# Optimization experiments

Measured on AMD Instinct MI355X. Metric: run time of the kernel, lower is better.

The kernel has to match this reference:

```python
import jax, jax.numpy as jnp
import numpy as np

B, S, H, A = 32, 2048, 1024, 256
NEG = jnp.float32(-1e20)


def setup_inputs() -> dict:
    key = jax.random.key(0)
    k = jax.random.split(key, 6)
    h_i = jax.random.normal(k[0], (B, S, H), jnp.float32)
    h_t = jax.random.normal(k[1], (B, H), jnp.float32)
    mask = jax.random.randint(k[2], (B, S), 0, 2).astype(bool)
    W = jax.random.normal(k[3], (A, 2 * H), jnp.float32) * 0.02
    b = jax.random.normal(k[4], (A,), jnp.float32) * 0.02
    u = jax.random.normal(k[5], (A, 1), jnp.float32)
    return {"h_i": h_i, "h_t": h_t, "mask": mask, "W": W, "b": b, "u": u}


def reference(h_i, h_t, mask, W, b, u):
    Bn, Sn, Hn = h_i.shape
    # h_t expanded along seq and concatenated: [B,S,2H]
    h_t_e = jnp.broadcast_to(h_t[:, None, :], (Bn, Sn, Hn))
    comb = jnp.concatenate([h_i, h_t_e], axis=-1)
    m = jnp.tanh(jnp.einsum('bsk,ak->bsa', comb, W) + b)  # [B,S,A]
    y = jnp.einsum('bsa,a->bs', m, u[:, 0])                # raw scores [B,S]
    # Faithful replication of torch masked_scatter per time step over the batch
    # dim: at step s, the masked batch positions receive SUCCESSIVE elements of
    # the score column y[:, s] (not necessarily the positionally aligned ones).
    pos = jnp.clip(jnp.cumsum(mask.astype(jnp.int32), axis=0) - 1, 0)  # [B,S]
    y_scattered = jnp.take_along_axis(y, pos, axis=0)
    beta = jnp.where(mask, y_scattered, NEG)
    alpha = jax.nn.softmax(beta, axis=1)                   # softmax over seq
    s = jnp.einsum('bs,bsh->bh', alpha, h_i)               # weighted sum [B,H]
    return s
```

## Files before the change

kernel.cpp:

```cpp
#include <hip/hip_runtime.h>
#include <math.h>

#define BB 32
#define SS 2048
#define HH 1024
#define AA 256
#define NEGV (-1e20f)
#define BK 32
#define NT (HH / BK)
#define NG 16

typedef _Float16 half8 __attribute__((ext_vector_type(8)));
typedef float f32x4 __attribute__((ext_vector_type(4)));

__device__ inline void async_lds16(const void* g, void* l) {
    __builtin_amdgcn_global_load_lds(
        (const __attribute__((address_space(1))) unsigned int*)g,
        (__attribute__((address_space(3))) unsigned int*)l, 16, 0, 0);
}

__device__ inline f32x4 gload4(const float* p) {
    f32x4 r;
    asm volatile("global_load_dwordx4 %0, %1, off"
                 : "=&v"(r) : "v"(p) : "memory");
    return r;
}

__device__ inline half8 cvt8(f32x4 a, f32x4 b) {
    half8 h;
    h[0] = (_Float16)a[0]; h[1] = (_Float16)a[1];
    h[2] = (_Float16)a[2]; h[3] = (_Float16)a[3];
    h[4] = (_Float16)b[0]; h[5] = (_Float16)b[1];
    h[6] = (_Float16)b[2]; h[7] = (_Float16)b[3];
    return h;
}
__device__ inline half8 cvt8f(float4 a, float4 b) {
    half8 h;
    h[0] = (_Float16)a.x; h[1] = (_Float16)a.y;
    h[2] = (_Float16)a.z; h[3] = (_Float16)a.w;
    h[4] = (_Float16)b.x; h[5] = (_Float16)b.y;
    h[6] = (_Float16)b.z; h[7] = (_Float16)b.w;
    return h;
}

__global__ __launch_bounds__(256) void k_prep(const float* __restrict__ W,
                                              const float* __restrict__ h_t,
                                              const float* __restrict__ bias,
                                              const int* __restrict__ mask,
                                              _Float16* __restrict__ W16t,
                                              float* __restrict__ c,
                                              int* __restrict__ sList,
                                              int* __restrict__ cntb,
                                              int* __restrict__ pcnt) {
    const int blk = blockIdx.x;
    const int tid = threadIdx.x;
    __shared__ int lcnt;

    if (blk < 128) {
        int idx = blk * 256 + tid;
        int kt = idx >> 10;
        int u  = idx & 1023;
        int col = u >> 2, ks = u & 3;
        const float* src = W + (size_t)col * 2 * HH + kt * BK + ks * 8;
        float4 a0 = *(const float4*)src;
        float4 a1 = *(const float4*)(src + 4);
        *reinterpret_cast<half8*>(W16t + (size_t)idx * 8) = cvt8f(a0, a1);
        return;
    }
    if (blk < 2176) {
        int wave = tid >> 6;
        int lane = tid & 63;
        int pair = (blk - 128) * 4 + wave;
        int b = pair >> 8;
        int a = pair & (AA - 1);
        const float* ht = h_t + (size_t)b * HH;
        const float* w2 = W + (size_t)a * 2 * HH + HH;
        float acc = 0.f;
        for (int k = lane; k < HH; k += 64)
            acc += ht[k] * w2[k];
        for (int off = 32; off; off >>= 1)
            acc += __shfl_down(acc, off, 64);
        if (lane == 0) c[pair] = acc + bias[a];
        return;
    }
    const int b = blk - 2176;
    const int lane = tid & 63;
    if (tid == 0) lcnt = 0;
    __syncthreads();
    int* lst = sList + b * SS;
#pragma unroll
    for (int i = 0; i < 8; ++i) {
        int s = tid + i * 256;
        int pref = 0, tot = 0;
#pragma unroll
        for (int bb = 0; bb < BB; ++bb) {
            int mv = (mask[bb * SS + s] != 0);
            tot += mv;
            if (bb <= b) pref += mv;
        }
        pcnt[b * SS + s] = pref;
        bool need = (tot > b);
        unsigned long long mk = __ballot(need);
        int wbase = 0;
        if (lane == 0) wbase = atomicAdd(&lcnt, __popcll(mk));
        wbase = __shfl(wbase, 0, 64);
        if (need) lst[wbase + __popcll(mk & ((1ull << lane) - 1))] = s;
    }
    __syncthreads();
    const int m = lcnt;
    if (tid == 0) cntb[b] = m;
    if (m > 0) {
        int padded = (m + 63) & ~63;
        int first = lst[0];
        for (int j = m + tid; j < padded; j += 256) lst[j] = first;
    }
}

__global__ __launch_bounds__(256, 3) void k2_mfma(const float* __restrict__ h_i,
                                                  const _Float16* __restrict__ W16t,
                                                  const float* __restrict__ c,
                                                  const float* __restrict__ u,
                                                  const int* __restrict__ sList,
                                                  const int* __restrict__ cntb,
                                                  float* __restrict__ y) {
    __shared__ _Float16 Alds[3][4][64][8];
    __shared__ _Float16 Blds[2][1024][8];
    __shared__ float c_s[AA], u_s[AA];
    __shared__ float red[2][64];
    __shared__ int s_idx[64];

    const int t = blockIdx.x;
    int b = -1, ti = 0, base = 0;
    for (int bb = 0; bb < BB; ++bb) {
        int nt = (cntb[bb] + 63) >> 6;
        if (b < 0 && t < base + nt) { b = bb; ti = t - base; }
        base += nt;
    }
    if (b < 0) return;

    const int tid = threadIdx.x;
    const int lane = tid & 63;
    const int wave = tid >> 6;
    const int wr = wave >> 1;
    const int wc = wave & 1;

    if (tid < 64) s_idx[tid] = sList[b * SS + ti * 64 + tid];
    c_s[tid] = c[b * AA + tid];
    u_s[tid] = u[tid];
    __syncthreads();

    f32x4 acc[2][8];
#pragma unroll
    for (int rf = 0; rf < 2; ++rf)
#pragma unroll
        for (int cf = 0; cf < 8; ++cf) acc[rf][cf] = (f32x4){0.f, 0.f, 0.f, 0.f};

    const int arow = tid >> 2;
    const int aks = tid & 3;
    const float* Abase = h_i + ((size_t)b * SS + s_idx[arow]) * HH + aks * 8;

    const int sb0 = __builtin_amdgcn_readfirstlane(wave * 256);
    _Float16* Bflat = &Blds[0][0][0];

    const int kq = lane >> 4;
    const int lr = lane & 15;

    f32x4 r0a = gload4(Abase);
    f32x4 r0b = gload4(Abase + 4);
    f32x4 r1a = gload4(Abase + BK);
    f32x4 r1b = gload4(Abase + BK + 4);
#pragma unroll
    for (int i = 0; i < 4; ++i) {
        int sbase = sb0 + i * 64;
        async_lds16(W16t + (size_t)(sbase + lane) * 8, Bflat + (size_t)sbase * 8);
    }
    f32x4 rAa = gload4(Abase + 2 * BK);
    f32x4 rAb = gload4(Abase + 2 * BK + 4);

    asm volatile("s_waitcnt vmcnt(6)" ::: "memory");
    __builtin_amdgcn_sched_barrier(0);
    *reinterpret_cast<half8*>(&Alds[0][aks][arow][0]) = cvt8(r0a, r0b);
    *reinterpret_cast<half8*>(&Alds[1][aks][arow][0]) = cvt8(r1a, r1b);
    asm volatile("s_waitcnt vmcnt(2) lgkmcnt(0)" ::: "memory");
    __builtin_amdgcn_sched_barrier(0);
    __builtin_amdgcn_s_barrier();

    for (int t2 = 0; t2 < NT; ++t2) {
        const int cur3 = t2 % 3, curB = t2 & 1;
        if (t2 + 1 < NT) {
#pragma unroll
            for (int i = 0; i < 4; ++i) {
                int sbase = sb0 + i * 64;
                async_lds16(W16t + (size_t)(t2 + 1) * 8192 + (size_t)(sbase + lane) * 8,
                            Bflat + (size_t)((t2 + 1) & 1) * 8192 + (size_t)sbase * 8);
            }
        }
        if (t2 + 2 < NT) {
            asm volatile("s_waitcnt vmcnt(4)" ::: "memory");
            __builtin_amdgcn_sched_barrier(0);
            *reinterpret_cast<half8*>(&Alds[(t2 + 2) % 3][aks][arow][0]) = cvt8(rAa, rAb);
        }
        if (t2 + 3 < NT) {
            rAa = gload4(Abase + (t2 + 3) * BK);
            rAb = gload4(Abase + (t2 + 3) * BK + 4);
        }
        half8 af[2], bf[8];
#pragma unroll
        for (int rf = 0; rf < 2; ++rf)
            af[rf] = *reinterpret_cast<half8*>(&Alds[cur3][kq][wr * 32 + rf * 16 + lr][0]);
#pragma unroll
        for (int cf = 0; cf < 8; ++cf) {
            int col = wc * 128 + cf * 16 + lr;
            bf[cf] = *reinterpret_cast<half8*>(
                Bflat + (size_t)curB * 8192 + (size_t)(col * 4 + kq) * 8);
        }
#pragma unroll
        for (int rf = 0; rf < 2; ++rf)
#pragma unroll
            for (int cf = 0; cf < 8; ++cf)
                acc[rf][cf] = __builtin_amdgcn_mfma_f32_16x16x32_f16(
                    af[rf], bf[cf], acc[rf][cf], 0, 0, 0);
        if (t2 < NT - 1) {
            if (t2 + 3 < NT)
                asm volatile("s_waitcnt vmcnt(2) lgkmcnt(0)" ::: "memory");
            else
                asm volatile("s_waitcnt vmcnt(0) lgkmcnt(0)" ::: "memory");
            __builtin_amdgcn_sched_barrier(0);
            __builtin_amdgcn_s_barrier();
        }
    }

#pragma unroll
    for (int rf = 0; rf < 2; ++rf) {
#pragma unroll
        for (int j = 0; j < 4; ++j) {
            float v = 0.f;
#pragma unroll
            for (int cf = 0; cf < 8; ++cf) {
                int col = wc * 128 + cf * 16 + lr;
                float z = acc[rf][cf][j] + c_s[col];
                v += tanhf(z) * u_s[col];
            }
            v += __shfl_xor(v, 1, 64);
            v += __shfl_xor(v, 2, 64);
            v += __shfl_xor(v, 4, 64);
            v += __shfl_xor(v, 8, 64);
            if (lr == 0) red[wc][wr * 32 + rf * 16 + kq * 4 + j] = v;
        }
    }
    __syncthreads();
    if (tid < 64) y[(size_t)b * SS + s_idx[tid]] = red[0][tid] + red[1][tid];
}

__global__ __launch_bounds__(256) void k34(const float* __restrict__ h_i,
                                           const float* __restrict__ y,
                                           const int* __restrict__ mask,
                                           const int* __restrict__ pcnt,
                                           float* __restrict__ partial) {
    const int blk = blockIdx.x;
    const int b = blk >> 4;
    const int grp = blk & (NG - 1);
    const int tid = threadIdx.x;
    const int lane = tid & 63;
    const int wave = tid >> 6;
    __shared__ float rmax[4], rsum[4];
    __shared__ float aval[128];
    __shared__ int slist[128];
    __shared__ int mtot;

    float beta[8];
    float mx = -INFINITY;
#pragma unroll
    for (int i = 0; i < 8; ++i) {
        int s = tid + i * 256;
        int p = pcnt[b * SS + s] - 1; if (p < 0) p = 0;
        float v = (mask[b * SS + s] != 0) ? y[(size_t)p * SS + s] : NEGV;
        beta[i] = v;
        mx = fmaxf(mx, v);
    }
    for (int off = 32; off; off >>= 1) mx = fmaxf(mx, __shfl_xor(mx, off, 64));
    if (lane == 0) rmax[wave] = mx;
    __syncthreads();
    mx = fmaxf(fmaxf(rmax[0], rmax[1]), fmaxf(rmax[2], rmax[3]));
    float sum = 0.f;
#pragma unroll
    for (int i = 0; i < 8; ++i) sum += expf(beta[i] - mx);
    for (int off = 32; off; off >>= 1) sum += __shfl_xor(sum, off, 64);
    if (lane == 0) rsum[wave] = sum;
    __syncthreads();
    sum = rsum[0] + rsum[1] + rsum[2] + rsum[3];
    const float inv = 1.f / sum;

    if (wave == 0) {
        int base = 0;
#pragma unroll
        for (int cc = 0; cc < 4; ++cc) {
            int s = grp * 128 + cc * 32 + lane;
            float a = 0.f;
            bool nz = false;
            if (lane < 32 && mask[b * SS + s] != 0) {
                int p = pcnt[b * SS + s] - 1; if (p < 0) p = 0;
                a = expf(y[(size_t)p * SS + s] - mx) * inv;
                nz = (a != 0.f);
            }
            unsigned long long mk = __ballot(nz);
            if (nz) {
                int off = base + __popcll(mk & ((1ull << lane) - 1));
                slist[off] = s;
                aval[off] = a;
            }
            base += __popcll(mk);
        }
        if (lane == 0) mtot = base;
    }
    __syncthreads();

    const int m = mtot;
    const float* basep = h_i + (size_t)b * SS * HH;
    f32x4 a0 = {0,0,0,0}, a1 = {0,0,0,0}, a2 = {0,0,0,0}, a3 = {0,0,0,0};
    int i2 = 0;
    for (; i2 + 4 <= m; i2 += 4) {
        float w0 = aval[i2],     w1 = aval[i2 + 1];
        float w2 = aval[i2 + 2], w3 = aval[i2 + 3];
        float4 v0 = *reinterpret_cast<const float4*>(&basep[(size_t)slist[i2]     * HH + tid * 4]);
        float4 v1 = *reinterpret_cast<const float4*>(&basep[(size_t)slist[i2 + 1] * HH + tid * 4]);
        float4 v2 = *reinterpret_cast<const float4*>(&basep[(size_t)slist[i2 + 2] * HH + tid * 4]);
        float4 v3 = *reinterpret_cast<const float4*>(&basep[(size_t)slist[i2 + 3] * HH + tid * 4]);
        a0[0] += w0 * v0.x; a0[1] += w0 * v0.y; a0[2] += w0 * v0.z; a0[3] += w0 * v0.w;
        a1[0] += w1 * v1.x; a1[1] += w1 * v1.y; a1[2] += w1 * v1.z; a1[3] += w1 * v1.w;
        a2[0] += w2 * v2.x; a2[1] += w2 * v2.y; a2[2] += w2 * v2.z; a2[3] += w2 * v2.w;
        a3[0] += w3 * v3.x; a3[1] += w3 * v3.y; a3[2] += w3 * v3.z; a3[3] += w3 * v3.w;
    }
    for (; i2 < m; ++i2) {
        float w0 = aval[i2];
        float4 v0 = *reinterpret_cast<const float4*>(&basep[(size_t)slist[i2] * HH + tid * 4]);
        a0[0] += w0 * v0.x; a0[1] += w0 * v0.y; a0[2] += w0 * v0.z; a0[3] += w0 * v0.w;
    }
    f32x4 acc4;
    acc4[0] = (a0[0] + a1[0]) + (a2[0] + a3[0]);
    acc4[1] = (a0[1] + a1[1]) + (a2[1] + a3[1]);
    acc4[2] = (a0[2] + a1[2]) + (a2[2] + a3[2]);
    acc4[3] = (a0[3] + a1[3]) + (a2[3] + a3[3]);
    *reinterpret_cast<f32x4*>(&partial[(size_t)blk * HH + tid * 4]) = acc4;
}

__global__ __launch_bounds__(256) void k4b_reduce(const float* __restrict__ partial,
                                                  float* __restrict__ out) {
    int i = blockIdx.x * 256 + threadIdx.x;
    int b = i >> 10, h = i & (HH - 1);
    float s = 0.f;
#pragma unroll
    for (int g = 0; g < NG; ++g)
        s += partial[((size_t)(b * NG + g)) * HH + h];
    out[i] = s;
}

extern "C" void kernel_launch(void* const* d_in, const int* in_sizes, int n_in,
                              void* d_out, int out_size, void* d_ws, size_t ws_size,
                              hipStream_t stream) {
    const float* h_i  = (const float*)d_in[0];
    const float* h_t  = (const float*)d_in[1];
    const int*   mask = (const int*)d_in[2];
    const float* W    = (const float*)d_in[3];
    const float* bias = (const float*)d_in[4];
    const float* u    = (const float*)d_in[5];
    float* out = (float*)d_out;

    float* c        = (float*)d_ws;
    float* y        = c + BB * AA;
    float* partial  = y + BB * SS;
    _Float16* W16t  = (_Float16*)(partial + BB * NG * HH);
    int* sList      = (int*)(W16t + AA * HH);
    int* cntb       = sList + BB * SS;
    int* pcnt       = cntb + BB;

    k_prep<<<2208, 256, 0, stream>>>(W, h_t, bias, mask, W16t, c, sList, cntb, pcnt);
    k2_mfma<<<1024, 256, 0, stream>>>(h_i, W16t, c, u, sList, cntb, y);
    k34<<<BB * NG, 256, 0, stream>>>(h_i, y, mask, pcnt, partial);
    k4b_reduce<<<(BB * HH) / 256, 256, 0, stream>>>(partial, out);
}
```

Measured before the change: 97.02 us.

## Replace partial-sum reduce kernel with float atomics and add MFMA priority hints

The final reduction kernel goes away. Each k34 block now atomically adds its partial weighted sum straight into the output, and the output is zeroed by extra blocks added to the prep kernel. This removes one kernel launch and the write and re-read of the partial buffer. The MFMA loop is also wrapped in s_setprio to raise wave priority during matrix ops. Atomics make the summation order nondeterministic and can cause contention with 16 blocks per output row.

```diff
diff --git a/kernel.cpp b/kernel.cpp
--- a/kernel.cpp
+++ b/kernel.cpp
@@ -51,7 +51,8 @@
                                               float* __restrict__ c,
                                               int* __restrict__ sList,
                                               int* __restrict__ cntb,
-                                              int* __restrict__ pcnt) {
+                                              int* __restrict__ pcnt,
+                                              float* __restrict__ out) {
     const int blk = blockIdx.x;
     const int tid = threadIdx.x;
     __shared__ int lcnt;
@@ -83,6 +84,11 @@
         if (lane == 0) c[pair] = acc + bias[a];
         return;
     }
+    if (blk >= 2208) {
+        int i = (blk - 2208) * 256 + tid;
+        *reinterpret_cast<f32x4*>(&out[(size_t)i * 4]) = (f32x4){0.f, 0.f, 0.f, 0.f};
+        return;
+    }
     const int b = blk - 2176;
     const int lane = tid & 63;
     if (tid == 0) lcnt = 0;
@@ -214,12 +220,14 @@
             bf[cf] = *reinterpret_cast<half8*>(
                 Bflat + (size_t)curB * 8192 + (size_t)(col * 4 + kq) * 8);
         }
+        __builtin_amdgcn_s_setprio(1);
 #pragma unroll
         for (int rf = 0; rf < 2; ++rf)
 #pragma unroll
             for (int cf = 0; cf < 8; ++cf)
                 acc[rf][cf] = __builtin_amdgcn_mfma_f32_16x16x32_f16(
                     af[rf], bf[cf], acc[rf][cf], 0, 0, 0);
+        __builtin_amdgcn_s_setprio(0);
         if (t2 < NT - 1) {
             if (t2 + 3 < NT)
                 asm volatile("s_waitcnt vmcnt(2) lgkmcnt(0)" ::: "memory");
@@ -256,7 +264,7 @@
                                            const float* __restrict__ y,
                                            const int* __restrict__ mask,
                                            const int* __restrict__ pcnt,
-                                           float* __restrict__ partial) {
+                                           float* __restrict__ out) {
     const int blk = blockIdx.x;
     const int b = blk >> 4;
     const int grp = blk & (NG - 1);
@@ -336,23 +344,15 @@
         float4 v0 = *reinterpret_cast<const float4*>(&basep[(size_t)slist[i2] * HH + tid * 4]);
         a0[0] += w0 * v0.x; a0[1] += w0 * v0.y; a0[2] += w0 * v0.z; a0[3] += w0 * v0.w;
     }
-    f32x4 acc4;
-    acc4[0] = (a0[0] + a1[0]) + (a2[0] + a3[0]);
-    acc4[1] = (a0[1] + a1[1]) + (a2[1] + a3[1]);
-    acc4[2] = (a0[2] + a1[2]) + (a2[2] + a3[2]);
-    acc4[3] = (a0[3] + a1[3]) + (a2[3] + a3[3]);
-    *reinterpret_cast<f32x4*>(&partial[(size_t)blk * HH + tid * 4]) = acc4;
-}
-
-__global__ __launch_bounds__(256) void k4b_reduce(const float* __restrict__ partial,
-                                                  float* __restrict__ out) {
-    int i = blockIdx.x * 256 + threadIdx.x;
-    int b = i >> 10, h = i & (HH - 1);
-    float s = 0.f;
-#pragma unroll
-    for (int g = 0; g < NG; ++g)
-        s += partial[((size_t)(b * NG + g)) * HH + h];
-    out[i] = s;
+    float r0 = (a0[0] + a1[0]) + (a2[0] + a3[0]);
+    float r1 = (a0[1] + a1[1]) + (a2[1] + a3[1]);
+    float r2 = (a0[2] + a1[2]) + (a2[2] + a3[2]);
+    float r3 = (a0[3] + a1[3]) + (a2[3] + a3[3]);
+    float* op = out + (size_t)b * HH + tid * 4;
+    unsafeAtomicAdd(op + 0, r0);
+    unsafeAtomicAdd(op + 1, r1);
+    unsafeAtomicAdd(op + 2, r2);
+    unsafeAtomicAdd(op + 3, r3);
 }
 
 extern "C" void kernel_launch(void* const* d_in, const int* in_sizes, int n_in,
@@ -368,14 +368,12 @@
 
     float* c        = (float*)d_ws;
     float* y        = c + BB * AA;
-    float* partial  = y + BB * SS;
-    _Float16* W16t  = (_Float16*)(partial + BB * NG * HH);
+    _Float16* W16t  = (_Float16*)(y + BB * SS);
     int* sList      = (int*)(W16t + AA * HH);
     int* cntb       = sList + BB * SS;
     int* pcnt       = cntb + BB;
 
-    k_prep<<<2208, 256, 0, stream>>>(W, h_t, bias, mask, W16t, c, sList, cntb, pcnt);
+    k_prep<<<2240, 256, 0, stream>>>(W, h_t, bias, mask, W16t, c, sList, cntb, pcnt, out);
     k2_mfma<<<1024, 256, 0, stream>>>(h_i, W16t, c, u, sList, cntb, y);
-    k34<<<BB * NG, 256, 0, stream>>>(h_i, y, mask, pcnt, partial);
-    k4b_reduce<<<(BB * HH) / 256, 256, 0, stream>>>(partial, out);
-}
+    k34<<<BB * NG, 256, 0, stream>>>(h_i, y, mask, pcnt, out);
+}
```

Result: no change. 97.91 us (+0.9%).
